# Performance work log

Hardware: AMD Instinct MI355X
Metric: run time of the kernel (lower is better)

The kernel has to match this reference:

```python
import jax, jax.numpy as jnp
import numpy as np
from jax import lax

B, C, H, W, K = 16, 64, 192, 192, 11
EPS = 1e-5


def _depthwise(x, w, pad):
    # x: (B,C,h,w), w: (C,1,kh,kw), pad: ((ph,ph),(pw,pw))
    return lax.conv_general_dilated(
        x, w, window_strides=(1, 1), padding=pad,
        feature_group_count=x.shape[1],
        dimension_numbers=('NCHW', 'OIHW', 'NCHW'))


def _maxpool3(x):
    return lax.reduce_window(x, -jnp.inf, lax.max,
                             (1, 1, 3, 3), (1, 1, 1, 1),
                             ((0, 0), (0, 0), (1, 1), (1, 1)))


def _blurpool(x):
    # filt_size=4, stride=3, reflect pad (1,2) on each spatial dim
    a = jnp.array([1., 3., 3., 1.], dtype=x.dtype)
    f = a[:, None] * a[None, :]
    f = f / f.sum()
    filt = jnp.tile(f[None, None], (x.shape[1], 1, 1, 1))  # (C,1,4,4)
    xp = jnp.pad(x, ((0, 0), (0, 0), (1, 2), (1, 2)), mode='reflect')
    return lax.conv_general_dilated(
        xp, filt, window_strides=(3, 3), padding='VALID',
        feature_group_count=x.shape[1],
        dimension_numbers=('NCHW', 'OIHW', 'NCHW'))


def _h_transform(x):
    b, c, h, w = x.shape
    x = jnp.pad(x, ((0, 0), (0, 0), (0, 0), (0, w)))
    x = x.reshape(b, c, -1)[..., :-w]
    return x.reshape(b, c, h, 2 * w - 1)


def _inv_h_transform(x):
    b, c, h, l = x.shape
    x = x.reshape(b, c, -1)
    x = jnp.pad(x, ((0, 0), (0, 0), (0, h)))
    x = x.reshape(b, c, h, 2 * h)
    return x[..., :h]


def _v_transform(x):
    return _h_transform(x.transpose(0, 1, 3, 2)).transpose(0, 1, 3, 2)


def _inv_v_transform(x):
    return _inv_h_transform(x.transpose(0, 1, 3, 2)).transpose(0, 1, 3, 2)


def _mra(x, w_h1, w_v1, w_h2, w_v2, bn_gamma, bn_beta, bn_mean, bn_var):
    kp = K // 2
    x_tem = _blurpool(_maxpool3(x))                 # (B,C,h,h), h=64
    x_h1 = _depthwise(x_tem, w_h1, ((kp, kp), (1, 1)))
    x_w1 = _depthwise(x_tem, w_v1, ((1, 1), (kp, kp)))
    x_h2 = _inv_h_transform(_depthwise(_h_transform(x_tem), w_h2, ((kp, kp), (1, 1))))
    x_w2 = _inv_v_transform(_depthwise(_v_transform(x_tem), w_v2, ((1, 1), (kp, kp))))
    att = x_h1 + x_w1 + x_h2 + x_w2
    # inference-mode BatchNorm2d
    inv = bn_gamma / jnp.sqrt(bn_var + EPS)
    att = att * inv[None, :, None, None] + (bn_beta - bn_mean * inv)[None, :, None, None]
    gate = jax.nn.sigmoid(att)                      # (B,C,h,h)
    # nearest-neighbor upsample to (H,W): torch idx = floor(i*h/H)
    h = gate.shape[-2]
    ih = (jnp.arange(H) * h) // H
    iw = (jnp.arange(W) * gate.shape[-1]) // W
    gate_up = gate[:, :, ih][:, :, :, iw]           # (B,C,H,W)
    return x[:, :C] * gate_up


def setup_inputs() -> dict:
    key = jax.random.key(0)
    ks = jax.random.split(key, 9)
    x = jax.random.normal(ks[0], (B, C, H, W), jnp.float32)
    w_h1 = jax.random.normal(ks[1], (C, 1, K, 3), jnp.float32) * 0.05
    w_v1 = jax.random.normal(ks[2], (C, 1, 3, K), jnp.float32) * 0.05
    w_h2 = jax.random.normal(ks[3], (C, 1, K, 3), jnp.float32) * 0.05
    w_v2 = jax.random.normal(ks[4], (C, 1, 3, K), jnp.float32) * 0.05
    bn_gamma = jnp.ones((C,), jnp.float32)
    bn_beta = jnp.zeros((C,), jnp.float32)
    bn_mean = jax.random.normal(ks[5], (C,), jnp.float32) * 0.1
    bn_var = jax.random.uniform(ks[6], (C,), jnp.float32, 0.5, 1.5)
    return {'x': x, 'w_h1': w_h1, 'w_v1': w_v1, 'w_h2': w_h2, 'w_v2': w_v2,
            'bn_gamma': bn_gamma, 'bn_beta': bn_beta,
            'bn_mean': bn_mean, 'bn_var': bn_var}


def reference(x, w_h1, w_v1, w_h2, w_v2, bn_gamma, bn_beta, bn_mean, bn_var):
    return _mra(x, w_h1, w_v1, w_h2, w_v2, bn_gamma, bn_beta, bn_mean, bn_var)
```

## Files before the change

kernel.cpp:

```cpp
#include <hip/hip_runtime.h>
#include <math.h>

__global__ __launch_bounds__(512, 8) void mra_fused(
    const float* __restrict__ x,
    const float* __restrict__ wh1g, const float* __restrict__ wv1g,
    const float* __restrict__ wh2g, const float* __restrict__ wv2g,
    const float* __restrict__ gamma, const float* __restrict__ beta,
    const float* __restrict__ mean, const float* __restrict__ var,
    float* __restrict__ out) {
    const int plane = blockIdx.x;
    const int c = plane & 63;
    __shared__ float T[64 * 80];
    __shared__ float gateL[64 * 64];

    const int j = threadIdx.x & 63;
    const int il = threadIdx.x >> 6;
    const int ib = il * 8;

    {
        float4 z4 = make_float4(0.f, 0.f, 0.f, 0.f);
        float4* t4 = (float4*)(T + ib * 80);
#pragma unroll
        for (int u = 0; u < 3; ++u) {
            int idx = u * 64 + j;
            if (idx < 160) t4[idx] = z4;
        }
    }

    const float* xp = x + (size_t)plane * 36864;

    {
        int colk[6];
#pragma unroll
        for (int k = 0; k < 6; ++k)
            colk[k] = min(max(3 * j - 2 + k, 0), 191);

        float rw[6][6];
#pragma unroll
        for (int s = 0; s < 6; ++s) {
            const float* rp = xp + (size_t)min(max(3 * ib - 2 + s, 0), 191) * 192;
#pragma unroll
            for (int k = 0; k < 6; ++k) rw[s][k] = rp[colk[k]];
        }

#define POOL_EMIT(I, S0, S1, S2, S3, S4, S5)                              \
        {                                                                 \
            float cbv[4];                                                 \
            {                                                             \
                float vmu[4][6];                                          \
                _Pragma("unroll") for (int k = 0; k < 6; ++k) {           \
                    float p0 = rw[S0][k], p1 = rw[S1][k], p2 = rw[S2][k]; \
                    float p3 = rw[S3][k], p4 = rw[S4][k], p5 = rw[S5][k]; \
                    float q1 = fmaxf(p1, p2), q2 = fmaxf(p2, p3);         \
                    float q3 = fmaxf(p3, p4), q4 = fmaxf(p4, p5);         \
                    vmu[0][k] = fmaxf(p0, q1);                            \
                    vmu[1][k] = fmaxf(p1, q2);                            \
                    vmu[2][k] = fmaxf(p2, q3);                            \
                    vmu[3][k] = fmaxf(p3, q4);                            \
                }                                                         \
                _Pragma("unroll") for (int u = 0; u < 4; ++u) {           \
                    float g1 = fmaxf(vmu[u][1], vmu[u][2]);               \
                    float g2 = fmaxf(vmu[u][2], vmu[u][3]);               \
                    float g3 = fmaxf(vmu[u][3], vmu[u][4]);               \
                    float g4 = fmaxf(vmu[u][4], vmu[u][5]);               \
                    float h0 = fmaxf(vmu[u][0], g1);                      \
                    float h1 = fmaxf(vmu[u][1], g2);                      \
                    float h2 = fmaxf(vmu[u][2], g3);                      \
                    float h3 = fmaxf(vmu[u][3], g4);                      \
                    float ha = (j == 0) ? h2 : h0;       \
                    cbv[u] = ha + 3.f * h1 + 3.f * h2 + h3;               \
                }                                                         \
            }                                                             \
            float c0 = ((I) == 0) ? cbv[2] : cbv[0];     \
            float accv = c0 + 3.f * cbv[1] + 3.f * cbv[2] + cbv[3];       \
            T[(I) * 80 + 6 + j] = accv * (1.f / 64.f);                    \
        }

#define LOAD3(BR, S0, S1, S2)                                             \
        {                                                                 \
            const float* rp0 = xp + (size_t)min((BR), 191) * 192;         \
            const float* rp1 = xp + (size_t)min((BR) + 1, 191) * 192;     \
            const float* rp2 = xp + (size_t)min((BR) + 2, 191) * 192;     \
            _Pragma("unroll") for (int k = 0; k < 6; ++k) {               \
                rw[S0][k] = rp0[colk[k]];                                 \
                rw[S1][k] = rp1[colk[k]];                                 \
                rw[S2][k] = rp2[colk[k]];                                 \
            }                                                             \
        }

#pragma unroll 1
        for (int ii = 0; ii < 8; ii += 2) {
            const int i = ib + ii;
            POOL_EMIT(i, 0, 1, 2, 3, 4, 5);
            LOAD3(3 * i + 4, 0, 1, 2);
            POOL_EMIT(i + 1, 3, 4, 5, 0, 1, 2);
            if (ii < 6) LOAD3(3 * i + 7, 3, 4, 5);
        }
#undef POOL_EMIT
#undef LOAD3
    }
    __syncthreads();

    const float inv = gamma[c] * rsqrtf(var[c] + 1e-5f);
    const float bias = beta[c] - mean[c] * inv;
    const int t0 = ib - 6;

    float Wa[33], Wb[33];
    float racc[13];

#pragma unroll
    for (int k = 0; k < 33; ++k) {
        Wa[k] = wh1g[c * 33 + k];
        Wb[k] = wh2g[c * 33 + k];
    }
#pragma unroll
    for (int k = 0; k < 13; ++k) racc[k] = 0.f;
#pragma unroll
    for (int tt = 0; tt < 20; ++tt) {
        const int t = t0 + tt;
        if (t >= 0 && t < 64) {
            float w_[13];
#pragma unroll
            for (int d = 0; d < 13; ++d) w_[d] = T[t * 80 + j + d];
#pragma unroll
            for (int p = 0; p < 11; ++p) {
                racc[(tt + 11 - p) % 13] +=
                    Wa[p * 3 + 0] * w_[5] + Wa[p * 3 + 1] * w_[6] +
                    Wa[p * 3 + 2] * w_[7] +
                    Wb[p * 3 + 0] * w_[10 - p] +
                    Wb[p * 3 + 1] * w_[11 - p] +
                    Wb[p * 3 + 2] * w_[12 - p];
            }
        }
        if (tt >= 12) gateL[(ib + tt - 12) * 64 + j] = racc[tt % 13];
        racc[tt % 13] = 0.f;
    }

    int g0s[3], rs[3];
#pragma unroll
    for (int u = 0; u < 3; ++u) {
        int m = j + 64 * u;
        int c4 = m % 48;
        int jj = 4 * c4;
        g0s[u] = jj / 3;
        rs[u] = jj - 3 * (jj / 3);
    }

#pragma unroll
    for (int k = 0; k < 33; ++k) {
        Wa[k] = wv1g[c * 33 + k];
        Wb[k] = wv2g[c * 33 + k];
    }
#pragma unroll
    for (int k = 0; k < 13; ++k) racc[k] = 0.f;
    const float4* xp4 = (const float4*)xp;
    float4* op4 = (float4*)(out + (size_t)plane * 36864);
#pragma unroll
    for (int tt = 0; tt < 20; ++tt) {
        const int t = t0 + tt;
        if (t >= 0 && t < 64) {
            float w_[13];
#pragma unroll
            for (int d = 0; d < 13; ++d) w_[d] = T[t * 80 + j + d];
#pragma unroll
            for (int p = 0; p < 3; ++p) {
#pragma unroll
                for (int q = 0; q < 11; ++q) {
                    racc[(tt + 7 - p) % 13] += Wa[p * 11 + q] * w_[q + 1];
                    racc[(tt + 2 - p + q) % 13] += Wb[p * 11 + q] * w_[q + 1];
                }
            }
        }
        if (tt >= 12) {
            const int i = ib + tt - 12;
            const int fb = i * 144;
            float4 xv0 = xp4[fb + j];
            float4 xv1 = xp4[fb + 64 + j];
            float4 xv2;
            if (j < 16) xv2 = xp4[fb + 128 + j];
            float z = (gateL[i * 64 + j] + racc[tt % 13]) * inv + bias;
            float g = 1.f / (1.f + __expf(-z));
            gateL[i * 64 + j] = g;
            const float* gr = gateL + i * 64;
            {
                float ga = gr[g0s[0]], gb = gr[g0s[0] + 1];
                float4 o;
                o.x = xv0.x * ga;
                o.y = xv0.y * (rs[0] == 2 ? gb : ga);
                o.z = xv0.z * (rs[0] == 0 ? ga : gb);
                o.w = xv0.w * gb;
                op4[fb + j] = o;
            }
            {
                float ga = gr[g0s[1]], gb = gr[g0s[1] + 1];
                float4 o;
                o.x = xv1.x * ga;
                o.y = xv1.y * (rs[1] == 2 ? gb : ga);
                o.z = xv1.z * (rs[1] == 0 ? ga : gb);
                o.w = xv1.w * gb;
                op4[fb + 64 + j] = o;
            }
            if (j < 16) {
                float ga = gr[g0s[2]], gb = gr[g0s[2] + 1];
                float4 o;
                o.x = xv2.x * ga;
                o.y = xv2.y * (rs[2] == 2 ? gb : ga);
                o.z = xv2.z * (rs[2] == 0 ? ga : gb);
                o.w = xv2.w * gb;
                op4[fb + 128 + j] = o;
            }
        }
        racc[tt % 13] = 0.f;
    }
}

extern "C" void kernel_launch(void* const* d_in, const int* in_sizes, int n_in,
                              void* d_out, int out_size, void* d_ws, size_t ws_size,
                              hipStream_t stream) {
    const float* x     = (const float*)d_in[0];
    const float* wh1   = (const float*)d_in[1];
    const float* wv1   = (const float*)d_in[2];
    const float* wh2   = (const float*)d_in[3];
    const float* wv2   = (const float*)d_in[4];
    const float* gamma = (const float*)d_in[5];
    const float* beta  = (const float*)d_in[6];
    const float* mean  = (const float*)d_in[7];
    const float* var   = (const float*)d_in[8];
    float* out  = (float*)d_out;

    mra_fused<<<1024, 512, 0, stream>>>(x, wh1, wv1, wh2, wv2,
                                        gamma, beta, mean, var, out);
}
```

Before: 297.0 us.

## Fuse horizontal and vertical conv passes and broadcast gate via wave shuffles

The two separate passes over the pooled tile (horizontal convs, then vertical convs) are merged into one pass, so each row of T is read from LDS once and all four weight sets stay in registers. The gateL shared-memory buffer is removed: the gate value is computed per lane and broadcast to neighbouring output columns with __shfl across the 64-wide wavefront. This cuts LDS traffic and shared memory footprint but raises register pressure (132 weight registers plus accumulators), which may lower occupancy or cause spills under the 512x8 launch bounds.

```diff
diff --git a/kernel.cpp b/kernel.cpp
--- a/kernel.cpp
+++ b/kernel.cpp
@@ -11,7 +11,6 @@
     const int plane = blockIdx.x;
     const int c = plane & 63;
     __shared__ float T[64 * 80];
-    __shared__ float gateL[64 * 64];
 
     const int j = threadIdx.x & 63;
     const int il = threadIdx.x >> 6;
@@ -105,35 +104,13 @@
     const float bias = beta[c] - mean[c] * inv;
     const int t0 = ib - 6;
 
-    float Wa[33], Wb[33];
-    float racc[13];
-
+    float Wh1[33], Wh2[33], Wv1[33], Wv2[33];
 #pragma unroll
     for (int k = 0; k < 33; ++k) {
-        Wa[k] = wh1g[c * 33 + k];
-        Wb[k] = wh2g[c * 33 + k];
-    }
-#pragma unroll
-    for (int k = 0; k < 13; ++k) racc[k] = 0.f;
-#pragma unroll
-    for (int tt = 0; tt < 20; ++tt) {
-        const int t = t0 + tt;
-        if (t >= 0 && t < 64) {
-            float w_[13];
-#pragma unroll
-            for (int d = 0; d < 13; ++d) w_[d] = T[t * 80 + j + d];
-#pragma unroll
-            for (int p = 0; p < 11; ++p) {
-                racc[(tt + 11 - p) % 13] +=
-                    Wa[p * 3 + 0] * w_[5] + Wa[p * 3 + 1] * w_[6] +
-                    Wa[p * 3 + 2] * w_[7] +
-                    Wb[p * 3 + 0] * w_[10 - p] +
-                    Wb[p * 3 + 1] * w_[11 - p] +
-                    Wb[p * 3 + 2] * w_[12 - p];
-            }
-        }
-        if (tt >= 12) gateL[(ib + tt - 12) * 64 + j] = racc[tt % 13];
-        racc[tt % 13] = 0.f;
+        Wh1[k] = wh1g[c * 33 + k];
+        Wh2[k] = wh2g[c * 33 + k];
+        Wv1[k] = wv1g[c * 33 + k];
+        Wv2[k] = wv2g[c * 33 + k];
     }
 
     int g0s[3], rs[3];
@@ -146,15 +123,13 @@
         rs[u] = jj - 3 * (jj / 3);
     }
 
-#pragma unroll
-    for (int k = 0; k < 33; ++k) {
-        Wa[k] = wv1g[c * 33 + k];
-        Wb[k] = wv2g[c * 33 + k];
-    }
+    float racc[13];
 #pragma unroll
     for (int k = 0; k < 13; ++k) racc[k] = 0.f;
+
     const float4* xp4 = (const float4*)xp;
     float4* op4 = (float4*)(out + (size_t)plane * 36864);
+
 #pragma unroll
     for (int tt = 0; tt < 20; ++tt) {
         const int t = t0 + tt;
@@ -163,11 +138,20 @@
 #pragma unroll
             for (int d = 0; d < 13; ++d) w_[d] = T[t * 80 + j + d];
 #pragma unroll
+            for (int p = 0; p < 11; ++p) {
+                racc[(tt + 11 - p) % 13] +=
+                    Wh1[p * 3 + 0] * w_[5] + Wh1[p * 3 + 1] * w_[6] +
+                    Wh1[p * 3 + 2] * w_[7] +
+                    Wh2[p * 3 + 0] * w_[10 - p] +
+                    Wh2[p * 3 + 1] * w_[11 - p] +
+                    Wh2[p * 3 + 2] * w_[12 - p];
+            }
+#pragma unroll
             for (int p = 0; p < 3; ++p) {
 #pragma unroll
                 for (int q = 0; q < 11; ++q) {
-                    racc[(tt + 7 - p) % 13] += Wa[p * 11 + q] * w_[q + 1];
-                    racc[(tt + 2 - p + q) % 13] += Wb[p * 11 + q] * w_[q + 1];
+                    racc[(tt + 7 - p) % 13] += Wv1[p * 11 + q] * w_[q + 1];
+                    racc[(tt + 2 - p + q) % 13] += Wv2[p * 11 + q] * w_[q + 1];
                 }
             }
         }
@@ -178,35 +162,33 @@
             float4 xv1 = xp4[fb + 64 + j];
             float4 xv2;
             if (j < 16) xv2 = xp4[fb + 128 + j];
-            float z = (gateL[i * 64 + j] + racc[tt % 13]) * inv + bias;
+            float z = racc[tt % 13] * inv + bias;
             float g = 1.f / (1.f + __expf(-z));
-            gateL[i * 64 + j] = g;
-            const float* gr = gateL + i * 64;
+            float ga0 = __shfl(g, g0s[0]), gb0 = __shfl(g, g0s[0] + 1);
+            float ga1 = __shfl(g, g0s[1]), gb1 = __shfl(g, g0s[1] + 1);
+            float ga2 = __shfl(g, g0s[2]), gb2 = __shfl(g, g0s[2] + 1);
             {
-                float ga = gr[g0s[0]], gb = gr[g0s[0] + 1];
                 float4 o;
-                o.x = xv0.x * ga;
-                o.y = xv0.y * (rs[0] == 2 ? gb : ga);
-                o.z = xv0.z * (rs[0] == 0 ? ga : gb);
-                o.w = xv0.w * gb;
+                o.x = xv0.x * ga0;
+                o.y = xv0.y * (rs[0] == 2 ? gb0 : ga0);
+                o.z = xv0.z * (rs[0] == 0 ? ga0 : gb0);
+                o.w = xv0.w * gb0;
                 op4[fb + j] = o;
             }
             {
-                float ga = gr[g0s[1]], gb = gr[g0s[1] + 1];
                 float4 o;
-                o.x = xv1.x * ga;
-                o.y = xv1.y * (rs[1] == 2 ? gb : ga);
-                o.z = xv1.z * (rs[1] == 0 ? ga : gb);
-                o.w = xv1.w * gb;
+                o.x = xv1.x * ga1;
+                o.y = xv1.y * (rs[1] == 2 ? gb1 : ga1);
+                o.z = xv1.z * (rs[1] == 0 ? ga1 : gb1);
+                o.w = xv1.w * gb1;
                 op4[fb + 64 + j] = o;
             }
             if (j < 16) {
-                float ga = gr[g0s[2]], gb = gr[g0s[2] + 1];
                 float4 o;
-                o.x = xv2.x * ga;
-                o.y = xv2.y * (rs[2] == 2 ? gb : ga);
-                o.z = xv2.z * (rs[2] == 0 ? ga : gb);
-                o.w = xv2.w * gb;
+                o.x = xv2.x * ga2;
+                o.y = xv2.y * (rs[2] == 2 ? gb2 : ga2);
+                o.z = xv2.z * (rs[2] == 0 ? ga2 : gb2);
+                o.w = xv2.w * gb2;
                 op4[fb + 128 + j] = o;
             }
         }
```

New measurement: 301.2 us. About the same (+1.4%).
